# Kernel optimization log

Measured on AMD Instinct MI355X. Metric: run time of the kernel, lower is better.

Reference implementation:

```python
import jax, jax.numpy as jnp
import numpy as np


def setup_inputs() -> dict:
    key = jax.random.key(0)
    ks = jax.random.split(key, 5)
    b, f, h, w, c = 2, 16, 64, 64, 256
    heads, D = 8, 32
    hD = heads * D
    x = jax.random.normal(ks[0], (b, f, h, w, c), dtype=jnp.float32)
    s = 1.0 / np.sqrt(c)
    Wq = jax.random.normal(ks[1], (c, hD), dtype=jnp.float32) * s
    Wk = jax.random.normal(ks[2], (c, hD), dtype=jnp.float32) * s
    Wv = jax.random.normal(ks[3], (c, hD), dtype=jnp.float32) * s
    Wo = jax.random.normal(ks[4], (hD, c), dtype=jnp.float32) * s
    return {"x": x, "Wq": Wq, "Wk": Wk, "Wv": Wv, "Wo": Wo, "heads": heads}


def reference(x, Wq, Wk, Wv, Wo, heads):
    b, f, h, w, c = x.shape
    hD = Wq.shape[1]
    D = hD // heads
    n = h * w
    # fuse batch & frames; 1x1 conv == channel matmul
    xf = x.reshape(b * f, n, c)  # [(bf), n, c]

    def proj(W):
        # [(bf), n, hD] -> [(bf), heads, D, n]
        p = jnp.einsum('bnc,cd->bnd', xf, W)
        return p.reshape(b * f, n, heads, D).transpose(0, 2, 3, 1)

    q = jax.nn.softmax(proj(Wq), axis=-2)  # softmax over D (note: scale is dead code in source)
    k = jax.nn.softmax(proj(Wk), axis=-1)  # softmax over spatial n
    v = proj(Wv)
    context = jnp.einsum('bhdn,bhen->bhde', k, v)      # [(bf), heads, D, D]
    out = jnp.einsum('bhde,bhdn->bhen', context, q)    # [(bf), heads, D, n]
    out = out.transpose(0, 3, 1, 2).reshape(b * f, n, hD)
    out = jnp.einsum('bnd,dc->bnc', out, Wo)
    return out.reshape(b, f, h, w, c)
```

## Files before the change

kernel.cpp:

```cpp
#include <hip/hip_runtime.h>
#include <hip/hip_bf16.h>


typedef __attribute__((ext_vector_type(8))) short bf16x8;
typedef __attribute__((ext_vector_type(4))) float f32x4;

__device__ __forceinline__ unsigned short f2bf(float x) {
  __hip_bfloat16 h = __float2bfloat16(x);
  union { __hip_bfloat16 b; unsigned short u; } c; c.b = h; return c.u;
}

__global__ __launch_bounds__(256) void k0_prep(const float* __restrict__ Wq,
                                               const float* __restrict__ Wk,
                                               const float* __restrict__ Wv,
                                               unsigned short* __restrict__ WqT,
                                               unsigned short* __restrict__ WkvT) {
  int r = blockIdx.x, c = threadIdx.x;
  if (r < 256)      WqT [(r      )*256 + c] = f2bf(Wq[c*256 + r]);
  else if (r < 512) WkvT[(r - 256)*256 + c] = f2bf(Wk[c*256 + (r-256)]);
  else              WkvT[(r - 256)*256 + c] = f2bf(Wv[c*256 + (r-512)]);
}

__global__ __launch_bounds__(1024, 4) void k1w(const float* __restrict__ x,
                                               const unsigned short* __restrict__ WkvT,
                                               float* __restrict__ ctxp) {
  __shared__ unsigned short As[2][32*256];
  __shared__ unsigned short slab[2][512*32];
  int bid = blockIdx.x;
  size_t rowbase = (size_t)bid * 256;
  int tid = threadIdx.x;
  int lane = tid & 63, w = tid >> 6;
  int cl = lane & 15, rq = (lane >> 4) << 2, fs = lane >> 4;
  int h = w & 7;
  bool isV = w >= 8;

  bf16x8 bfr[2][8];
#pragma unroll
  for (int ni = 0; ni < 2; ++ni)
#pragma unroll
    for (int kk = 0; kk < 8; ++kk)
      bfr[ni][kk] = *(const bf16x8*)(WkvT + (size_t)(w*32 + ni*16 + cl)*256 + kk*32 + fs*8);

  f32x4 c2[2] = {};
  float dena0 = 0.f, dena1 = 0.f;

  int ar = tid >> 5, as_ = tid & 31;
  int aw = ar*256 + ((as_ ^ (ar & 7)) << 3);
  const float* ap = x + (rowbase + ar)*256 + as_*8;

  int ca0 = h*32 + cl, ca1 = h*32 + 16 + cl;
  int cb  = 256 + h*32 + (isV ? 16 : 0) + cl;
  int ra0 = ca0*32 + ((fs ^ ((ca0 ^ (ca0 >> 2)) & 3)) << 3);
  int ra1 = ca1*32 + ((fs ^ ((ca1 ^ (ca1 >> 2)) & 3)) << 3);
  int rb  = cb*32  + ((fs ^ ((cb  ^ (cb  >> 2)) & 3)) << 3);

  f32x4 acc[2][2];

  float4 pa0 = *(const float4*)ap;
  float4 pa1 = *(const float4*)(ap + 4);
  {
    unsigned short* Ab = &As[0][0];
    union { ushort4 u4[2]; int4 i4; } pk;
    pk.u4[0].x = f2bf(pa0.x); pk.u4[0].y = f2bf(pa0.y); pk.u4[0].z = f2bf(pa0.z); pk.u4[0].w = f2bf(pa0.w);
    pk.u4[1].x = f2bf(pa1.x); pk.u4[1].y = f2bf(pa1.y); pk.u4[1].z = f2bf(pa1.z); pk.u4[1].w = f2bf(pa1.w);
    *(int4*)(&Ab[aw]) = pk.i4;
  }
  {
    const float* apn = ap + 32*256;
    pa0 = *(const float4*)apn;
    pa1 = *(const float4*)(apn + 4);
  }
  __syncthreads();
  {
    unsigned short* Ab = &As[0][0];
#pragma unroll
    for (int m = 0; m < 2; ++m)
#pragma unroll
      for (int ni = 0; ni < 2; ++ni) acc[m][ni] = (f32x4){};
#pragma unroll
    for (int kk = 0; kk < 8; ++kk) {
      int so = (((kk*4 + fs) ^ (cl & 7)) << 3);
      bf16x8 a0 = *(const bf16x8*)(&Ab[cl*256 + so]);
      bf16x8 a1 = *(const bf16x8*)(&Ab[(16 + cl)*256 + so]);
#pragma unroll
      for (int ni = 0; ni < 2; ++ni) {
        acc[0][ni] = __builtin_amdgcn_mfma_f32_16x16x32_bf16(a0, bfr[ni][kk], acc[0][ni], 0, 0, 0);
        acc[1][ni] = __builtin_amdgcn_mfma_f32_16x16x32_bf16(a1, bfr[ni][kk], acc[1][ni], 0, 0, 0);
      }
    }
  }

  for (int t = 0; t < 7; ++t) {
    {
      unsigned short* sb = &slab[t & 1][0];
#pragma unroll
      for (int ni = 0; ni < 2; ++ni) {
        int c = w*32 + ni*16 + cl;
        int sw = (c ^ (c >> 2)) & 3;
#pragma unroll
        for (int m = 0; m < 2; ++m) {
          int n4 = m*16 + rq;
          ushort4 wv;
          if (!isV) {
            float e0 = __expf(acc[m][ni][0]), e1 = __expf(acc[m][ni][1]);
            float e2 = __expf(acc[m][ni][2]), e3 = __expf(acc[m][ni][3]);
            if (ni == 0) dena0 += (e0 + e1) + (e2 + e3); else dena1 += (e0 + e1) + (e2 + e3);
            wv.x = f2bf(e0); wv.y = f2bf(e1); wv.z = f2bf(e2); wv.w = f2bf(e3);
          } else {
            wv.x = f2bf(acc[m][ni][0]); wv.y = f2bf(acc[m][ni][1]);
            wv.z = f2bf(acc[m][ni][2]); wv.w = f2bf(acc[m][ni][3]);
          }
          *(ushort4*)(&sb[c*32 + (((n4 >> 3) ^ sw) << 3) + (n4 & 7)]) = wv;
        }
      }
    }
    {
      unsigned short* Ab = &As[(t + 1) & 1][0];
      union { ushort4 u4[2]; int4 i4; } pk;
      pk.u4[0].x = f2bf(pa0.x); pk.u4[0].y = f2bf(pa0.y); pk.u4[0].z = f2bf(pa0.z); pk.u4[0].w = f2bf(pa0.w);
      pk.u4[1].x = f2bf(pa1.x); pk.u4[1].y = f2bf(pa1.y); pk.u4[1].z = f2bf(pa1.z); pk.u4[1].w = f2bf(pa1.w);
      *(int4*)(&Ab[aw]) = pk.i4;
    }
    if (t < 6) {
      const float* apn = ap + (size_t)(t + 2)*32*256;
      pa0 = *(const float4*)apn;
      pa1 = *(const float4*)(apn + 4);
    }
    __syncthreads();
    {
      unsigned short* sb = &slab[t & 1][0];
      bf16x8 af0 = *(const bf16x8*)(&sb[ra0]);
      bf16x8 af1 = *(const bf16x8*)(&sb[ra1]);
      bf16x8 bv  = *(const bf16x8*)(&sb[rb]);
      c2[0] = __builtin_amdgcn_mfma_f32_16x16x32_bf16(af0, bv, c2[0], 0, 0, 0);
      c2[1] = __builtin_amdgcn_mfma_f32_16x16x32_bf16(af1, bv, c2[1], 0, 0, 0);
    }
    {
      unsigned short* Ab = &As[(t + 1) & 1][0];
#pragma unroll
      for (int m = 0; m < 2; ++m)
#pragma unroll
        for (int ni = 0; ni < 2; ++ni) acc[m][ni] = (f32x4){};
#pragma unroll
      for (int kk = 0; kk < 8; ++kk) {
        int so = (((kk*4 + fs) ^ (cl & 7)) << 3);
        bf16x8 a0 = *(const bf16x8*)(&Ab[cl*256 + so]);
        bf16x8 a1 = *(const bf16x8*)(&Ab[(16 + cl)*256 + so]);
#pragma unroll
        for (int ni = 0; ni < 2; ++ni) {
          acc[0][ni] = __builtin_amdgcn_mfma_f32_16x16x32_bf16(a0, bfr[ni][kk], acc[0][ni], 0, 0, 0);
          acc[1][ni] = __builtin_amdgcn_mfma_f32_16x16x32_bf16(a1, bfr[ni][kk], acc[1][ni], 0, 0, 0);
        }
      }
    }
  }
  {
    unsigned short* sb = &slab[1][0];
#pragma unroll
    for (int ni = 0; ni < 2; ++ni) {
      int c = w*32 + ni*16 + cl;
      int sw = (c ^ (c >> 2)) & 3;
#pragma unroll
      for (int m = 0; m < 2; ++m) {
        int n4 = m*16 + rq;
        ushort4 wv;
        if (!isV) {
          float e0 = __expf(acc[m][ni][0]), e1 = __expf(acc[m][ni][1]);
          float e2 = __expf(acc[m][ni][2]), e3 = __expf(acc[m][ni][3]);
          if (ni == 0) dena0 += (e0 + e1) + (e2 + e3); else dena1 += (e0 + e1) + (e2 + e3);
          wv.x = f2bf(e0); wv.y = f2bf(e1); wv.z = f2bf(e2); wv.w = f2bf(e3);
        } else {
          wv.x = f2bf(acc[m][ni][0]); wv.y = f2bf(acc[m][ni][1]);
          wv.z = f2bf(acc[m][ni][2]); wv.w = f2bf(acc[m][ni][3]);
        }
        *(ushort4*)(&sb[c*32 + (((n4 >> 3) ^ sw) << 3) + (n4 & 7)]) = wv;
      }
    }
  }
  __syncthreads();
  {
    unsigned short* sb = &slab[1][0];
    bf16x8 af0 = *(const bf16x8*)(&sb[ra0]);
    bf16x8 af1 = *(const bf16x8*)(&sb[ra1]);
    bf16x8 bv  = *(const bf16x8*)(&sb[rb]);
    c2[0] = __builtin_amdgcn_mfma_f32_16x16x32_bf16(af0, bv, c2[0], 0, 0, 0);
    c2[1] = __builtin_amdgcn_mfma_f32_16x16x32_bf16(af1, bv, c2[1], 0, 0, 0);
  }
  float* cp = ctxp + ((size_t)bid*8 + h)*1056;
  int ec = isV ? 16 + cl : cl;
#pragma unroll
  for (int di = 0; di < 2; ++di)
#pragma unroll
    for (int r = 0; r < 4; ++r)
      cp[(di*16 + rq + r)*33 + ec] = c2[di][r];
  if (!isV) {
    dena0 += __shfl_xor(dena0, 16); dena0 += __shfl_xor(dena0, 32);
    dena1 += __shfl_xor(dena1, 16); dena1 += __shfl_xor(dena1, 32);
    if (fs == 0) {
      cp[cl*33 + 32]        = dena0;
      cp[(16 + cl)*33 + 32] = dena1;
    }
  }
}

__global__ __launch_bounds__(256) void k2b_w2(const float* __restrict__ ctxp,
                                              const float* __restrict__ Wo,
                                              unsigned short* __restrict__ W2t) {
  __shared__ float clds[32*33];
  int bid = blockIdx.x;
  int h = bid & 7, bfi = bid >> 3;
  int tid = threadIdx.x;
  for (int i = tid; i < 1056; i += 256) {
    float s = 0.f;
#pragma unroll
    for (int p = 0; p < 16; ++p)
      s += ctxp[((size_t)(bfi*16 + p)*8 + h)*1056 + i];
    clds[i] = s;
  }
  __syncthreads();
  float acc[32] = {};
#pragma unroll 4
  for (int e = 0; e < 32; ++e) {
    float w = Wo[(size_t)(h*32 + e)*256 + tid];
#pragma unroll
    for (int d = 0; d < 32; ++d) acc[d] += clds[d*33 + e] * w;
  }
  unsigned short* o = W2t + ((size_t)bfi*256 + tid)*256 + h*32;
#pragma unroll
  for (int d = 0; d < 32; ++d) o[d] = f2bf(acc[d] / clds[d*33 + 32]);
}

__global__ __launch_bounds__(512, 2) void k3s(const float* __restrict__ x,
                                              const unsigned short* __restrict__ WqT,
                                              const unsigned short* __restrict__ W2t,
                                              float* __restrict__ out) {
  __shared__ unsigned short As[2][32*256];
  __shared__ unsigned short Qs[2][32*256];
  int bid = blockIdx.x;
  size_t rowbase = (size_t)bid * 256;
  int bfi = bid >> 4;
  int tid = threadIdx.x;
  int lane = tid & 63, wid = tid >> 6;
  int cl = lane & 15, rq = (lane >> 4) << 2, fs = lane >> 4;

  bf16x8 bq[2][8], bw[2][8];
#pragma unroll
  for (int nf = 0; nf < 2; ++nf)
#pragma unroll
    for (int kk = 0; kk < 8; ++kk) {
      bq[nf][kk] = *(const bf16x8*)(WqT + (size_t)(wid*32 + nf*16 + cl)*256 + kk*32 + fs*8);
      bw[nf][kk] = *(const bf16x8*)(W2t + ((size_t)bfi*256 + wid*32 + nf*16 + cl)*256 + kk*32 + fs*8);
    }

  int ar = tid >> 5, as_ = tid & 31;
  int aw0 = ar*256 + ((as_ ^ (ar & 7)) << 3);
  int aw1 = (16 + ar)*256 + ((as_ ^ (ar & 7)) << 3);
  const float* ap = x + (rowbase + ar)*256 + as_*8;

  int qslotbase = wid*4 + (rq >> 3);
  ushort4 qpk[2][2];

  float4 pa0 = *(const float4*)ap;
  float4 pa1 = *(const float4*)(ap + 4);
  float4 pa2 = *(const float4*)(ap + 16*256);
  float4 pa3 = *(const float4*)(ap + 16*256 + 4);
  {
    unsigned short* Ab = &As[0][0];
    union { ushort4 u4[2]; int4 i4; } pk;
    pk.u4[0].x = f2bf(pa0.x); pk.u4[0].y = f2bf(pa0.y); pk.u4[0].z = f2bf(pa0.z); pk.u4[0].w = f2bf(pa0.w);
    pk.u4[1].x = f2bf(pa1.x); pk.u4[1].y = f2bf(pa1.y); pk.u4[1].z = f2bf(pa1.z); pk.u4[1].w = f2bf(pa1.w);
    *(int4*)(&Ab[aw0]) = pk.i4;
    pk.u4[0].x = f2bf(pa2.x); pk.u4[0].y = f2bf(pa2.y); pk.u4[0].z = f2bf(pa2.z); pk.u4[0].w = f2bf(pa2.w);
    pk.u4[1].x = f2bf(pa3.x); pk.u4[1].y = f2bf(pa3.y); pk.u4[1].z = f2bf(pa3.z); pk.u4[1].w = f2bf(pa3.w);
    *(int4*)(&Ab[aw1]) = pk.i4;
  }
  {
    const float* apn = ap + 32*256;
    pa0 = *(const float4*)apn;
    pa1 = *(const float4*)(apn + 4);
    pa2 = *(const float4*)(apn + 16*256);
    pa3 = *(const float4*)(apn + 16*256 + 4);
  }
  __syncthreads();
  {
    unsigned short* Ab = &As[0][0];
    f32x4 ql[2][2] = {};
#pragma unroll
    for (int kk = 0; kk < 8; ++kk) {
      int so = (((kk*4 + fs) ^ (cl & 7)) << 3);
      bf16x8 a0 = *(const bf16x8*)(&Ab[cl*256 + so]);
      bf16x8 a1 = *(const bf16x8*)(&Ab[(16 + cl)*256 + so]);
#pragma unroll
      for (int nf = 0; nf < 2; ++nf) {
        ql[0][nf] = __builtin_amdgcn_mfma_f32_16x16x32_bf16(bq[nf][kk], a0, ql[0][nf], 0, 0, 0);
        ql[1][nf] = __builtin_amdgcn_mfma_f32_16x16x32_bf16(bq[nf][kk], a1, ql[1][nf], 0, 0, 0);
      }
    }
#pragma unroll
    for (int m = 0; m < 2; ++m) {
      float e0[4], e1[4]; float s8 = 0.f;
#pragma unroll
      for (int r = 0; r < 4; ++r) { e0[r] = __expf(ql[m][0][r]); e1[r] = __expf(ql[m][1][r]); s8 += e0[r] + e1[r]; }
      float s = s8; s += __shfl_xor(s, 16); s += __shfl_xor(s, 32);
      float inv = 1.0f / s;
      qpk[m][0].x = f2bf(e0[0]*inv); qpk[m][0].y = f2bf(e0[1]*inv); qpk[m][0].z = f2bf(e0[2]*inv); qpk[m][0].w = f2bf(e0[3]*inv);
      qpk[m][1].x = f2bf(e1[0]*inv); qpk[m][1].y = f2bf(e1[1]*inv); qpk[m][1].z = f2bf(e1[2]*inv); qpk[m][1].w = f2bf(e1[3]*inv);
    }
  }
  for (int t = 0; t < 7; ++t) {
    {
      unsigned short* Ab = &As[(t + 1) & 1][0];
      union { ushort4 u4[2]; int4 i4; } pk;
      pk.u4[0].x = f2bf(pa0.x); pk.u4[0].y = f2bf(pa0.y); pk.u4[0].z = f2bf(pa0.z); pk.u4[0].w = f2bf(pa0.w);
      pk.u4[1].x = f2bf(pa1.x); pk.u4[1].y = f2bf(pa1.y); pk.u4[1].z = f2bf(pa1.z); pk.u4[1].w = f2bf(pa1.w);
      *(int4*)(&Ab[aw0]) = pk.i4;
      pk.u4[0].x = f2bf(pa2.x); pk.u4[0].y = f2bf(pa2.y); pk.u4[0].z = f2bf(pa2.z); pk.u4[0].w = f2bf(pa2.w);
      pk.u4[1].x = f2bf(pa3.x); pk.u4[1].y = f2bf(pa3.y); pk.u4[1].z = f2bf(pa3.z); pk.u4[1].w = f2bf(pa3.w);
      *(int4*)(&Ab[aw1]) = pk.i4;
    }
    {
      unsigned short* Qb = &Qs[t & 1][0];
#pragma unroll
      for (int m = 0; m < 2; ++m) {
        int row = m*16 + cl;
#pragma unroll
        for (int nf = 0; nf < 2; ++nf) {
          int slot = qslotbase + nf*2;
          *(ushort4*)(&Qb[row*256 + ((slot ^ (row & 7)) << 3) + (rq & 4)]) = qpk[m][nf];
        }
      }
    }
    if (t < 6) {
      const float* apn = ap + (size_t)(t + 2)*32*256;
      pa0 = *(const float4*)apn;
      pa1 = *(const float4*)(apn + 4);
      pa2 = *(const float4*)(apn + 16*256);
      pa3 = *(const float4*)(apn + 16*256 + 4);
    }
    __syncthreads();
    f32x4 oa[2][2] = {};
    {
      unsigned short* Qb = &Qs[t & 1][0];
#pragma unroll
      for (int kk = 0; kk < 8; ++kk) {
        int so = (((kk*4 + fs) ^ (cl & 7)) << 3);
        bf16x8 q0 = *(const bf16x8*)(&Qb[cl*256 + so]);
        bf16x8 q1 = *(const bf16x8*)(&Qb[(16 + cl)*256 + so]);
#pragma unroll
        for (int nf = 0; nf < 2; ++nf) {
          oa[0][nf] = __builtin_amdgcn_mfma_f32_16x16x32_bf16(bw[nf][kk], q0, oa[0][nf], 0, 0, 0);
          oa[1][nf] = __builtin_amdgcn_mfma_f32_16x16x32_bf16(bw[nf][kk], q1, oa[1][nf], 0, 0, 0);
        }
      }
    }
    {
      unsigned short* Ab = &As[(t + 1) & 1][0];
      f32x4 ql[2][2] = {};
#pragma unroll
      for (int kk = 0; kk < 8; ++kk) {
        int so = (((kk*4 + fs) ^ (cl & 7)) << 3);
        bf16x8 a0 = *(const bf16x8*)(&Ab[cl*256 + so]);
        bf16x8 a1 = *(const bf16x8*)(&Ab[(16 + cl)*256 + so]);
#pragma unroll
        for (int nf = 0; nf < 2; ++nf) {
          ql[0][nf] = __builtin_amdgcn_mfma_f32_16x16x32_bf16(bq[nf][kk], a0, ql[0][nf], 0, 0, 0);
          ql[1][nf] = __builtin_amdgcn_mfma_f32_16x16x32_bf16(bq[nf][kk], a1, ql[1][nf], 0, 0, 0);
        }
      }
#pragma unroll
      for (int m = 0; m < 2; ++m) {
        float e0[4], e1[4]; float s8 = 0.f;
#pragma unroll
        for (int r = 0; r < 4; ++r) { e0[r] = __expf(ql[m][0][r]); e1[r] = __expf(ql[m][1][r]); s8 += e0[r] + e1[r]; }
        float s = s8; s += __shfl_xor(s, 16); s += __shfl_xor(s, 32);
        float inv = 1.0f / s;
        qpk[m][0].x = f2bf(e0[0]*inv); qpk[m][0].y = f2bf(e0[1]*inv); qpk[m][0].z = f2bf(e0[2]*inv); qpk[m][0].w = f2bf(e0[3]*inv);
        qpk[m][1].x = f2bf(e1[0]*inv); qpk[m][1].y = f2bf(e1[1]*inv); qpk[m][1].z = f2bf(e1[2]*inv); qpk[m][1].w = f2bf(e1[3]*inv);
      }
    }
#pragma unroll
    for (int m = 0; m < 2; ++m)
#pragma unroll
      for (int nf = 0; nf < 2; ++nf)
        *(f32x4*)(&out[(rowbase + (size_t)t*32 + m*16 + cl)*256 + wid*32 + nf*16 + rq]) = oa[m][nf];
  }
  {
    unsigned short* Qb = &Qs[1][0];
#pragma unroll
    for (int m = 0; m < 2; ++m) {
      int row = m*16 + cl;
#pragma unroll
      for (int nf = 0; nf < 2; ++nf) {
        int slot = qslotbase + nf*2;
        *(ushort4*)(&Qb[row*256 + ((slot ^ (row & 7)) << 3) + (rq & 4)]) = qpk[m][nf];
      }
    }
  }
  __syncthreads();
  {
    unsigned short* Qb = &Qs[1][0];
    f32x4 oa[2][2] = {};
#pragma unroll
    for (int kk = 0; kk < 8; ++kk) {
      int so = (((kk*4 + fs) ^ (cl & 7)) << 3);
      bf16x8 q0 = *(const bf16x8*)(&Qb[cl*256 + so]);
      bf16x8 q1 = *(const bf16x8*)(&Qb[(16 + cl)*256 + so]);
#pragma unroll
      for (int nf = 0; nf < 2; ++nf) {
        oa[0][nf] = __builtin_amdgcn_mfma_f32_16x16x32_bf16(bw[nf][kk], q0, oa[0][nf], 0, 0, 0);
        oa[1][nf] = __builtin_amdgcn_mfma_f32_16x16x32_bf16(bw[nf][kk], q1, oa[1][nf], 0, 0, 0);
      }
    }
#pragma unroll
    for (int m = 0; m < 2; ++m)
#pragma unroll
      for (int nf = 0; nf < 2; ++nf)
        *(f32x4*)(&out[(rowbase + (size_t)7*32 + m*16 + cl)*256 + wid*32 + nf*16 + rq]) = oa[m][nf];
  }
}

extern "C" void kernel_launch(void* const* d_in, const int* in_sizes, int n_in,
                              void* d_out, int out_size, void* d_ws, size_t ws_size,
                              hipStream_t stream) {
  const float* x  = (const float*)d_in[0];
  const float* Wq = (const float*)d_in[1];
  const float* Wk = (const float*)d_in[2];
  const float* Wv = (const float*)d_in[3];
  const float* Wo = (const float*)d_in[4];
  float* out = (float*)d_out;

  unsigned short* WkvT = (unsigned short*)d_ws;
  unsigned short* WqT  = WkvT + 131072;
  unsigned short* W2t  = WqT  + 65536;
  float*          ctxp = (float*)(W2t + 2097152);

  k0_prep <<<768,  256,  0, stream>>>(Wq, Wk, Wv, WqT, WkvT);
  k1w     <<<512,  1024, 0, stream>>>(x, WkvT, ctxp);
  k2b_w2  <<<256,  256,  0, stream>>>(ctxp, Wo, W2t);
  k3s     <<<512,  512,  0, stream>>>(x, WqT, W2t, out);
}
```

Baseline: 141.1 us.

## Cache bf16 copy of x in first pass and DMA it straight to LDS

The first kernel now also writes the bf16-converted x tiles it already builds to a workspace buffer. The output kernel reads that bf16 copy with direct global-to-LDS loads (global_load_lds), with the swizzle applied on the global address side. This removes the fp32 reloads, the conversions and the register staging from the second pass. Total bytes moved stay about the same (an extra 64MB write against a 64MB smaller read), and correctness depends on the async LDS loads being complete at each barrier.

Result: slower. 156.4 us (+10.8%).

```diff
diff --git a/kernel.cpp b/kernel.cpp
--- a/kernel.cpp
+++ b/kernel.cpp
@@ -8,6 +8,11 @@
 __device__ __forceinline__ unsigned short f2bf(float x) {
   __hip_bfloat16 h = __float2bfloat16(x);
   union { __hip_bfloat16 b; unsigned short u; } c; c.b = h; return c.u;
+}
+
+__device__ __forceinline__ void gl16(const unsigned short* g, unsigned short* l) {
+  __builtin_amdgcn_global_load_lds((const __attribute__((address_space(1))) void*)g,
+                                   (__attribute__((address_space(3))) void*)l, 16, 0, 0);
 }
 
 __global__ __launch_bounds__(256) void k0_prep(const float* __restrict__ Wq,
@@ -23,7 +28,8 @@
 
 __global__ __launch_bounds__(1024, 4) void k1w(const float* __restrict__ x,
                                                const unsigned short* __restrict__ WkvT,
-                                               float* __restrict__ ctxp) {
+                                               float* __restrict__ ctxp,
+                                               unsigned short* __restrict__ XB) {
   __shared__ unsigned short As[2][32*256];
   __shared__ unsigned short slab[2][512*32];
   int bid = blockIdx.x;
@@ -47,6 +53,7 @@
   int ar = tid >> 5, as_ = tid & 31;
   int aw = ar*256 + ((as_ ^ (ar & 7)) << 3);
   const float* ap = x + (rowbase + ar)*256 + as_*8;
+  unsigned short* xbp = XB + (rowbase + ar)*256 + as_*8;
 
   int ca0 = h*32 + cl, ca1 = h*32 + 16 + cl;
   int cb  = 256 + h*32 + (isV ? 16 : 0) + cl;
@@ -64,6 +71,7 @@
     pk.u4[0].x = f2bf(pa0.x); pk.u4[0].y = f2bf(pa0.y); pk.u4[0].z = f2bf(pa0.z); pk.u4[0].w = f2bf(pa0.w);
     pk.u4[1].x = f2bf(pa1.x); pk.u4[1].y = f2bf(pa1.y); pk.u4[1].z = f2bf(pa1.z); pk.u4[1].w = f2bf(pa1.w);
     *(int4*)(&Ab[aw]) = pk.i4;
+    *(int4*)xbp = pk.i4;
   }
   {
     const float* apn = ap + 32*256;
@@ -120,6 +128,7 @@
       pk.u4[0].x = f2bf(pa0.x); pk.u4[0].y = f2bf(pa0.y); pk.u4[0].z = f2bf(pa0.z); pk.u4[0].w = f2bf(pa0.w);
       pk.u4[1].x = f2bf(pa1.x); pk.u4[1].y = f2bf(pa1.y); pk.u4[1].z = f2bf(pa1.z); pk.u4[1].w = f2bf(pa1.w);
       *(int4*)(&Ab[aw]) = pk.i4;
+      *(int4*)(xbp + (size_t)(t + 1)*8192) = pk.i4;
     }
     if (t < 6) {
       const float* apn = ap + (size_t)(t + 2)*32*256;
@@ -230,7 +239,7 @@
   for (int d = 0; d < 32; ++d) o[d] = f2bf(acc[d] / clds[d*33 + 32]);
 }
 
-__global__ __launch_bounds__(512, 2) void k3s(const float* __restrict__ x,
+__global__ __launch_bounds__(512, 2) void k3x(const unsigned short* __restrict__ XB,
                                               const unsigned short* __restrict__ WqT,
                                               const unsigned short* __restrict__ W2t,
                                               float* __restrict__ out) {
@@ -252,38 +261,19 @@
       bw[nf][kk] = *(const bf16x8*)(W2t + ((size_t)bfi*256 + wid*32 + nf*16 + cl)*256 + kk*32 + fs*8);
     }
 
-  int ar = tid >> 5, as_ = tid & 31;
-  int aw0 = ar*256 + ((as_ ^ (ar & 7)) << 3);
-  int aw1 = (16 + ar)*256 + ((as_ ^ (ar & 7)) << 3);
-  const float* ap = x + (rowbase + ar)*256 + as_*8;
+  int sr = tid >> 5, ss = tid & 31;
+  const unsigned short* xs0 = XB + (rowbase + sr)*256 + ((ss ^ (sr & 7)) << 3);
+  const unsigned short* xs1 = xs0 + 16*256;
 
   int qslotbase = wid*4 + (rq >> 3);
   ushort4 qpk[2][2];
 
-  float4 pa0 = *(const float4*)ap;
-  float4 pa1 = *(const float4*)(ap + 4);
-  float4 pa2 = *(const float4*)(ap + 16*256);
-  float4 pa3 = *(const float4*)(ap + 16*256 + 4);
-  {
-    unsigned short* Ab = &As[0][0];
-    union { ushort4 u4[2]; int4 i4; } pk;
-    pk.u4[0].x = f2bf(pa0.x); pk.u4[0].y = f2bf(pa0.y); pk.u4[0].z = f2bf(pa0.z); pk.u4[0].w = f2bf(pa0.w);
-    pk.u4[1].x = f2bf(pa1.x); pk.u4[1].y = f2bf(pa1.y); pk.u4[1].z = f2bf(pa1.z); pk.u4[1].w = f2bf(pa1.w);
-    *(int4*)(&Ab[aw0]) = pk.i4;
-    pk.u4[0].x = f2bf(pa2.x); pk.u4[0].y = f2bf(pa2.y); pk.u4[0].z = f2bf(pa2.z); pk.u4[0].w = f2bf(pa2.w);
-    pk.u4[1].x = f2bf(pa3.x); pk.u4[1].y = f2bf(pa3.y); pk.u4[1].z = f2bf(pa3.z); pk.u4[1].w = f2bf(pa3.w);
-    *(int4*)(&Ab[aw1]) = pk.i4;
-  }
-  {
-    const float* apn = ap + 32*256;
-    pa0 = *(const float4*)apn;
-    pa1 = *(const float4*)(apn + 4);
-    pa2 = *(const float4*)(apn + 16*256);
-    pa3 = *(const float4*)(apn + 16*256 + 4);
-  }
-  __syncthreads();
-  {
-    unsigned short* Ab = &As[0][0];
+  auto stageA = [&](int buf, int ts) {
+    gl16(xs0 + (size_t)ts*8192, &As[buf][(wid*64)*8]);
+    gl16(xs1 + (size_t)ts*8192, &As[buf][(512 + wid*64)*8]);
+  };
+  auto p1soft = [&](int buf) {
+    unsigned short* Ab = &As[buf][0];
     f32x4 ql[2][2] = {};
 #pragma unroll
     for (int kk = 0; kk < 8; ++kk) {
@@ -306,37 +296,27 @@
       qpk[m][0].x = f2bf(e0[0]*inv); qpk[m][0].y = f2bf(e0[1]*inv); qpk[m][0].z = f2bf(e0[2]*inv); qpk[m][0].w = f2bf(e0[3]*inv);
       qpk[m][1].x = f2bf(e1[0]*inv); qpk[m][1].y = f2bf(e1[1]*inv); qpk[m][1].z = f2bf(e1[2]*inv); qpk[m][1].w = f2bf(e1[3]*inv);
     }
-  }
+  };
+  auto qwrite = [&](int buf) {
+    unsigned short* Qb = &Qs[buf][0];
+#pragma unroll
+    for (int m = 0; m < 2; ++m) {
+      int row = m*16 + cl;
+#pragma unroll
+      for (int nf = 0; nf < 2; ++nf) {
+        int slot = qslotbase + nf*2;
+        *(ushort4*)(&Qb[row*256 + ((slot ^ (row & 7)) << 3) + (rq & 4)]) = qpk[m][nf];
+      }
+    }
+  };
+
+  stageA(0, 0);
+  __syncthreads();
+  p1soft(0);
+
   for (int t = 0; t < 7; ++t) {
-    {
-      unsigned short* Ab = &As[(t + 1) & 1][0];
-      union { ushort4 u4[2]; int4 i4; } pk;
-      pk.u4[0].x = f2bf(pa0.x); pk.u4[0].y = f2bf(pa0.y); pk.u4[0].z = f2bf(pa0.z); pk.u4[0].w = f2bf(pa0.w);
-      pk.u4[1].x = f2bf(pa1.x); pk.u4[1].y = f2bf(pa1.y); pk.u4[1].z = f2bf(pa1.z); pk.u4[1].w = f2bf(pa1.w);
-      *(int4*)(&Ab[aw0]) = pk.i4;
-      pk.u4[0].x = f2bf(pa2.x); pk.u4[0].y = f2bf(pa2.y); pk.u4[0].z = f2bf(pa2.z); pk.u4[0].w = f2bf(pa2.w);
-      pk.u4[1].x = f2bf(pa3.x); pk.u4[1].y = f2bf(pa3.y); pk.u4[1].z = f2bf(pa3.z); pk.u4[1].w = f2bf(pa3.w);
-      *(int4*)(&Ab[aw1]) = pk.i4;
-    }
-    {
-      unsigned short* Qb = &Qs[t & 1][0];
-#pragma unroll
-      for (int m = 0; m < 2; ++m) {
-        int row = m*16 + cl;
-#pragma unroll
-        for (int nf = 0; nf < 2; ++nf) {
-          int slot = qslotbase + nf*2;
-          *(ushort4*)(&Qb[row*256 + ((slot ^ (row & 7)) << 3) + (rq & 4)]) = qpk[m][nf];
-        }
-      }
-    }
-    if (t < 6) {
-      const float* apn = ap + (size_t)(t + 2)*32*256;
-      pa0 = *(const float4*)apn;
-      pa1 = *(const float4*)(apn + 4);
-      pa2 = *(const float4*)(apn + 16*256);
-      pa3 = *(const float4*)(apn + 16*256 + 4);
-    }
+    stageA((t + 1) & 1, t + 1);
+    qwrite(t & 1);
     __syncthreads();
     f32x4 oa[2][2] = {};
     {
@@ -353,49 +333,14 @@
         }
       }
     }
-    {
-      unsigned short* Ab = &As[(t + 1) & 1][0];
-      f32x4 ql[2][2] = {};
-#pragma unroll
-      for (int kk = 0; kk < 8; ++kk) {
-        int so = (((kk*4 + fs) ^ (cl & 7)) << 3);
-        bf16x8 a0 = *(const bf16x8*)(&Ab[cl*256 + so]);
-        bf16x8 a1 = *(const bf16x8*)(&Ab[(16 + cl)*256 + so]);
-#pragma unroll
-        for (int nf = 0; nf < 2; ++nf) {
-          ql[0][nf] = __builtin_amdgcn_mfma_f32_16x16x32_bf16(bq[nf][kk], a0, ql[0][nf], 0, 0, 0);
-          ql[1][nf] = __builtin_amdgcn_mfma_f32_16x16x32_bf16(bq[nf][kk], a1, ql[1][nf], 0, 0, 0);
-        }
-      }
-#pragma unroll
-      for (int m = 0; m < 2; ++m) {
-        float e0[4], e1[4]; float s8 = 0.f;
-#pragma unroll
-        for (int r = 0; r < 4; ++r) { e0[r] = __expf(ql[m][0][r]); e1[r] = __expf(ql[m][1][r]); s8 += e0[r] + e1[r]; }
-        float s = s8; s += __shfl_xor(s, 16); s += __shfl_xor(s, 32);
-        float inv = 1.0f / s;
-        qpk[m][0].x = f2bf(e0[0]*inv); qpk[m][0].y = f2bf(e0[1]*inv); qpk[m][0].z = f2bf(e0[2]*inv); qpk[m][0].w = f2bf(e0[3]*inv);
-        qpk[m][1].x = f2bf(e1[0]*inv); qpk[m][1].y = f2bf(e1[1]*inv); qpk[m][1].z = f2bf(e1[2]*inv); qpk[m][1].w = f2bf(e1[3]*inv);
-      }
-    }
+    p1soft((t + 1) & 1);
 #pragma unroll
     for (int m = 0; m < 2; ++m)
 #pragma unroll
       for (int nf = 0; nf < 2; ++nf)
         *(f32x4*)(&out[(rowbase + (size_t)t*32 + m*16 + cl)*256 + wid*32 + nf*16 + rq]) = oa[m][nf];
   }
-  {
-    unsigned short* Qb = &Qs[1][0];
-#pragma unroll
-    for (int m = 0; m < 2; ++m) {
-      int row = m*16 + cl;
-#pragma unroll
-      for (int nf = 0; nf < 2; ++nf) {
-        int slot = qslotbase + nf*2;
-        *(ushort4*)(&Qb[row*256 + ((slot ^ (row & 7)) << 3) + (rq & 4)]) = qpk[m][nf];
-      }
-    }
-  }
+  qwrite(1);
   __syncthreads();
   {
     unsigned short* Qb = &Qs[1][0];
@@ -433,9 +378,10 @@
   unsigned short* WqT  = WkvT + 131072;
   unsigned short* W2t  = WqT  + 65536;
   float*          ctxp = (float*)(W2t + 2097152);
+  unsigned short* XB   = (unsigned short*)(ctxp + (size_t)512*8*1056);
 
   k0_prep <<<768,  256,  0, stream>>>(Wq, Wk, Wv, WqT, WkvT);
-  k1w     <<<512,  1024, 0, stream>>>(x, WkvT, ctxp);
+  k1w     <<<512,  1024, 0, stream>>>(x, WkvT, ctxp, XB);
   k2b_w2  <<<256,  256,  0, stream>>>(ctxp, Wo, W2t);
-  k3s     <<<512,  512,  0, stream>>>(x, WqT, W2t, out);
-}
+  k3x     <<<512,  512,  0, stream>>>(XB, WqT, W2t, out);
+}
```
